# Kernel tuning notes

Measured on AMD Instinct MI355X. Metric: run time of the kernel, lower is better.

The kernel has to match this reference:

```python
import jax, jax.numpy as jnp
import numpy as np

N_NODES = 100000
N_EDGES = 1600000
N_GRAPHS = 4096
IN_DIM, HID, OUT_DIM = 128, 128, 64
BN_EPS = 1e-5


def gcn_conv(x, W, b, src, dst):
    """PyG GCNConv: symmetric norm with self-loops. x:[N,Fin] -> [N,Fout]."""
    h = x @ W  # [N, Fout]
    ones = jnp.ones((src.shape[0],), dtype=h.dtype)
    deg = jax.ops.segment_sum(ones, dst, num_segments=N_NODES) + 1.0  # +1 for self-loop
    dinv = jax.lax.rsqrt(deg)  # deg >= 1, safe
    norm = dinv[src] * dinv[dst]  # [E]
    msg = h[src] * norm[:, None]  # [E, Fout] gather + scale
    agg = jax.ops.segment_sum(msg, dst, num_segments=N_NODES)
    agg = agg + h * (dinv * dinv)[:, None]  # self-loop term, norm = dinv_i^2
    return agg + b


def batchnorm(x, gamma, beta):
    mu = jnp.mean(x, axis=0)
    var = jnp.mean(jnp.square(x - mu), axis=0)  # biased var, torch BN training mode
    return (x - mu) * jax.lax.rsqrt(var + BN_EPS) * gamma + beta


def setup_inputs() -> dict:
    key = jax.random.key(0)
    ks = jax.random.split(key, 12)
    x = jax.random.normal(ks[0], (N_NODES, IN_DIM), dtype=jnp.float32)
    edge_index = jax.random.randint(ks[1], (2, N_EDGES), 0, N_NODES, dtype=jnp.int64)
    batch = jnp.sort(jax.random.randint(ks[2], (N_NODES,), 0, N_GRAPHS, dtype=jnp.int64))
    def lin(k, fi, fo):
        s = 1.0 / np.sqrt(fi)
        return jax.random.uniform(k, (fi, fo), jnp.float32, -s, s)
    return {
        "x": x, "edge_index": edge_index, "batch": batch,
        "W1": lin(ks[3], IN_DIM, HID), "b1": jnp.zeros((HID,), jnp.float32),
        "g1": jnp.ones((HID,), jnp.float32), "be1": jnp.zeros((HID,), jnp.float32),
        "W2": lin(ks[4], HID, HID), "b2": jnp.zeros((HID,), jnp.float32),
        "g2": jnp.ones((HID,), jnp.float32), "be2": jnp.zeros((HID,), jnp.float32),
        "W3": lin(ks[5], HID, HID), "b3": jnp.zeros((HID,), jnp.float32),
        "g3": jnp.ones((HID,), jnp.float32), "be3": jnp.zeros((HID,), jnp.float32),
        "fcW": lin(ks[6], HID, OUT_DIM),
        "fcb": jax.random.uniform(ks[7], (OUT_DIM,), jnp.float32, -1/np.sqrt(HID), 1/np.sqrt(HID)),
    }


def reference(x, edge_index, batch, W1, b1, g1, be1, W2, b2, g2, be2, W3, b3, g3, be3, fcW, fcb):
    src, dst = edge_index[0], edge_index[1]
    h = jax.nn.relu(batchnorm(gcn_conv(x, W1, b1, src, dst), g1, be1))
    h = jax.nn.relu(batchnorm(gcn_conv(h, W2, b2, src, dst), g2, be2))
    h = jax.nn.relu(batchnorm(gcn_conv(h, W3, b3, src, dst), g3, be3))
    # global mean pool over graphs
    sums = jax.ops.segment_sum(h, batch, num_segments=N_GRAPHS)  # [G, HID]
    cnt = jax.ops.segment_sum(jnp.ones((N_NODES,), h.dtype), batch, num_segments=N_GRAPHS)
    pooled = sums / jnp.maximum(cnt, 1.0)[:, None]
    return pooled @ fcW + fcb
```

## Files before the change

### kernel.cpp

```cpp
#include <hip/hip_runtime.h>

#define NN 100000
#define NE 1600000
#define NG 4096
#define HID 128
#define ODIM 64
#define BN_EPS 1e-5f
#define NBUK 782
#define BPAD 896
#define NZROW 256
#define CHUNK 16384
#define PREP_HIST 256
#define PREP_GOFF 17
#define PREP_W 192

typedef unsigned int u32;
typedef unsigned short u16;
typedef short short8 __attribute__((ext_vector_type(8)));
typedef float f32x4 __attribute__((ext_vector_type(4)));

__device__ inline u32 pack_bf16(float a, float b) {
  u32 ua = __float_as_uint(a), ub = __float_as_uint(b);
  ua += 0x7fffu + ((ua >> 16) & 1u);
  ub += 0x7fffu + ((ub >> 16) & 1u);
  return (ua >> 16) | (ub & 0xffff0000u);
}
__device__ inline u16 bf16_of(float v) {
  u32 ua = __float_as_uint(v);
  ua += 0x7fffu + ((ua >> 16) & 1u);
  return (u16)(ua >> 16);
}
__device__ inline float bf_lo(u32 u) { return __uint_as_float(u << 16); }
__device__ inline float bf_hi(u32 u) { return __uint_as_float(u & 0xffff0000u); }

__global__ __launch_bounds__(256) void k_prep(const int* __restrict__ ei, int* __restrict__ bcnt,
                                              const int* __restrict__ batch, int* __restrict__ goff,
                                              const float* __restrict__ W1, const float* __restrict__ W2,
                                              const float* __restrict__ W3, u16* __restrict__ Wt1,
                                              u16* __restrict__ Wt2, u16* __restrict__ Wt3) {
  __shared__ int h[NBUK];
  int b = blockIdx.x, t = threadIdx.x;
  if (b < PREP_HIST) {
    for (int i = t; i < NBUK; i += 256) h[i] = 0;
    __syncthreads();
    const int stride = PREP_HIST * 256;
    for (int e = b * 256 + t; e < NE; e += stride)
      atomicAdd(&h[ei[NE + e] >> 7], 1);
    __syncthreads();
    for (int i = t; i < NBUK; i += 256)
      if (h[i]) atomicAdd(&bcnt[i], h[i]);
  } else if (b < PREP_HIST + PREP_GOFF) {
    int g = (b - PREP_HIST) * 256 + t;
    if (g <= NG) {
      int lo = 0, hi = NN;
      while (lo < hi) { int mid = (lo + hi) >> 1; if (batch[mid] < g) lo = mid + 1; else hi = mid; }
      goff[g] = lo;
    }
  } else {
    int idx = (b - PREP_HIST - PREP_GOFF) * 256 + t;
    int mat = idx >> 14;
    int rem = idx & 16383;
    int n = rem >> 7, k = rem & 127;
    const float* W = (mat == 0) ? W1 : (mat == 1) ? W2 : W3;
    u16* Wt = (mat == 0) ? Wt1 : (mat == 1) ? Wt2 : Wt3;
    Wt[(n << 7) + k] = bf16_of(W[(k << 7) + n]);
  }
}

__global__ __launch_bounds__(1024) void k_bscan(const int* __restrict__ bcnt, int* __restrict__ bboff,
                                                int* __restrict__ bcur) {
  __shared__ int ls[1024];
  int t = threadIdx.x;
  ls[t] = (t < NBUK) ? bcnt[t] : 0;
  __syncthreads();
  for (int d = 1; d < 1024; d <<= 1) {
    int v = 0;
    if (t >= d) v = ls[t - d];
    __syncthreads();
    ls[t] += v;
    __syncthreads();
  }
  if (t < NBUK) {
    int ex = (t == 0) ? 0 : ls[t - 1];
    bboff[t] = ex;
    bcur[t] = ex;
  }
  if (t == 0) bboff[NBUK] = NE;
}

__global__ __launch_bounds__(1024) void k_bscatter(const int* __restrict__ ei, int* __restrict__ bcur,
                                                   u32* __restrict__ ebuf) {
  __shared__ int cnt[NBUK], rnk[NBUK], base[NBUK];
  int t = threadIdx.x;
  int e0 = blockIdx.x * CHUNK;
  for (int i = t; i < NBUK; i += 1024) { cnt[i] = 0; rnk[i] = 0; }
  __syncthreads();
  for (int i = t; i < CHUNK; i += 1024) {
    int e = e0 + i;
    if (e < NE) atomicAdd(&cnt[ei[NE + e] >> 7], 1);
  }
  __syncthreads();
  for (int i = t; i < NBUK; i += 1024) {
    int c = cnt[i];
    base[i] = c ? atomicAdd(&bcur[i], c) : 0;
  }
  __syncthreads();
  for (int i = t; i < CHUNK; i += 1024) {
    int e = e0 + i;
    if (e < NE) {
      int s = ei[e], d = ei[NE + e];
      int b = d >> 7;
      int r = atomicAdd(&rnk[b], 1);
      ebuf[base[b] + r] = ((u32)(d & 127) << 17) | (u32)s;
    }
  }
}

__global__ __launch_bounds__(256) void k_csr(const u32* __restrict__ ebuf, const int* __restrict__ bboff,
                                             int* __restrict__ off, int* __restrict__ oend,
                                             float* __restrict__ dinv, u32* __restrict__ csrc) {
  __shared__ int cnt[128], scn[128], cur[128];
  int b = blockIdx.x, t = threadIdx.x;
  int n0 = b << 7;
  int ebeg = bboff[b], eend = bboff[b + 1];
  int pboff = ebeg + BPAD * b;
  if (t < 128) cnt[t] = 0;
  __syncthreads();
  for (int e = ebeg + t; e < eend; e += 256) atomicAdd(&cnt[ebuf[e] >> 17], 1);
  __syncthreads();
  int pc = 0;
  if (t < 128) { pc = (cnt[t] + 7) & ~7; scn[t] = pc; }
  __syncthreads();
  for (int d = 1; d < 128; d <<= 1) {
    int v = 0;
    if (t >= d && t < 128) v = scn[t - d];
    __syncthreads();
    if (t < 128) scn[t] += v;
    __syncthreads();
  }
  int nvalid = min(128, NN - n0);
  if (t < 128) {
    int ex = scn[t] - pc;
    cur[t] = ex;
    if (t < nvalid) {
      off[n0 + t] = pboff + ex;
      oend[n0 + t] = pboff + scn[t];
      dinv[n0 + t] = rsqrtf((float)cnt[t] + 1.0f);
    }
  }
  __syncthreads();
  for (int e = ebeg + t; e < eend; e += 256) {
    u32 p = ebuf[e];
    int d = p >> 17;
    int pos = pboff + atomicAdd(&cur[d], 1);
    csrc[pos] = p & 0x1ffffu;
  }
  if (t < 128) {
    int ex = scn[t] - pc;
    for (int i = cnt[t]; i < pc; ++i)
      csrc[pboff + ex + i] = (u32)(NN + ((n0 + t + i) & (NZROW - 1)));
  }
}

__global__ __launch_bounds__(256) void k_gemm1(const float* __restrict__ A, const u16* __restrict__ Wt,
                                               const float* __restrict__ dinv, u16* __restrict__ H) {
  __shared__ u16 Ct[128][128];
  u16 (*At)[32] = (u16 (*)[32])(&Ct[0][0]);
  u16 (*Bt)[32] = (u16 (*)[32])(&Ct[32][0]);

  int t = threadIdx.x;
  int w = t >> 6, l = t & 63;
  int quad = l >> 4, lid = l & 15;
  int row0 = blockIdx.x * 128;

  f32x4 acc[2][8];
#pragma unroll
  for (int mt = 0; mt < 2; ++mt)
#pragma unroll
    for (int nt = 0; nt < 8; ++nt) acc[mt][nt] = (f32x4){0.f, 0.f, 0.f, 0.f};

  int ar = t >> 1;
  int ac = (t & 1) << 4;
  int grow = row0 + ar;
  bool aok = grow < NN;

  for (int k0 = 0; k0 < HID; k0 += 32) {
    float4 f0 = {0, 0, 0, 0}, f1 = {0, 0, 0, 0}, f2 = {0, 0, 0, 0}, f3 = {0, 0, 0, 0};
    if (aok) {
      const float4* ap = (const float4*)(A + (size_t)grow * HID + k0 + ac);
      f0 = ap[0]; f1 = ap[1]; f2 = ap[2]; f3 = ap[3];
    }
    uint4 q0, q1;
    q0.x = pack_bf16(f0.x, f0.y); q0.y = pack_bf16(f0.z, f0.w);
    q0.z = pack_bf16(f1.x, f1.y); q0.w = pack_bf16(f1.z, f1.w);
    q1.x = pack_bf16(f2.x, f2.y); q1.y = pack_bf16(f2.z, f2.w);
    q1.z = pack_bf16(f3.x, f3.y); q1.w = pack_bf16(f3.z, f3.w);
    *(uint4*)&At[ar][ac] = q0;
    *(uint4*)&At[ar][ac + 8] = q1;
    const u16* wp = Wt + (size_t)(t >> 1) * HID + k0 + ac;
    *(uint4*)&Bt[t >> 1][ac]     = ((const uint4*)wp)[0];
    *(uint4*)&Bt[t >> 1][ac + 8] = ((const uint4*)wp)[1];
    __syncthreads();
    short8 a0 = *(const short8*)&At[(w << 5) + lid][quad << 3];
    short8 a1 = *(const short8*)&At[(w << 5) + 16 + lid][quad << 3];
#pragma unroll
    for (int nt = 0; nt < 8; ++nt) {
      short8 b = *(const short8*)&Bt[(nt << 4) + lid][quad << 3];
      acc[0][nt] = __builtin_amdgcn_mfma_f32_16x16x32_bf16(a0, b, acc[0][nt], 0, 0, 0);
      acc[1][nt] = __builtin_amdgcn_mfma_f32_16x16x32_bf16(a1, b, acc[1][nt], 0, 0, 0);
    }
    __syncthreads();
  }

  int valid = min(128, NN - row0);
#pragma unroll
  for (int mt = 0; mt < 2; ++mt) {
#pragma unroll
    for (int r = 0; r < 4; ++r) {
      int rl = (w << 5) + (mt << 4) + (quad << 2) + r;
      float dv = (rl < valid) ? dinv[row0 + rl] : 0.f;
#pragma unroll
      for (int nt = 0; nt < 8; ++nt) {
        Ct[rl][(nt << 4) + lid] = bf16_of(acc[mt][nt][r] * dv);
      }
    }
  }
  __syncthreads();
  u16* Hb = H + (size_t)row0 * HID;
  int tot = valid << 4;
  for (int idx = t; idx < tot; idx += 256) {
    ((uint4*)Hb)[idx] = ((const uint4*)Ct)[idx];
  }
}

__device__ inline u32 bn_pair(u32 v, float2 sc, float2 sh) {
  float a = fmaxf(fmaf(bf_lo(v), sc.x, sh.x), 0.f);
  float b = fmaxf(fmaf(bf_hi(v), sc.y, sh.y), 0.f);
  return pack_bf16(a, b);
}

__global__ __launch_bounds__(256) void k_gemm_b(const u16* __restrict__ A, const u16* __restrict__ Wt,
                                                const float* __restrict__ sums, const float* __restrict__ g,
                                                const float* __restrict__ be,
                                                const float* __restrict__ dinv, u16* __restrict__ H) {
  __shared__ u16 Ct[128][128];
  u16 (*At)[32] = (u16 (*)[32])(&Ct[0][0]);
  u16 (*Bt)[32] = (u16 (*)[32])(&Ct[32][0]);
  float* scsh = (float*)&Ct[64][0];

  int t = threadIdx.x;
  int w = t >> 6, l = t & 63;
  int quad = l >> 4, lid = l & 15;
  int row0 = blockIdx.x * 128;

  if (t < 128) {
    const float invN = 1.0f / (float)NN;
    float mu = sums[t] * invN;
    float var = sums[HID + t] * invN - mu * mu;
    float sc = g[t] * rsqrtf(var + BN_EPS);
    scsh[t] = sc;
    scsh[128 + t] = be[t] - mu * sc;
  }

  f32x4 acc[2][8];
#pragma unroll
  for (int mt = 0; mt < 2; ++mt)
#pragma unroll
    for (int nt = 0; nt < 8; ++nt) acc[mt][nt] = (f32x4){0.f, 0.f, 0.f, 0.f};

  int ar = t >> 1;
  int ac = (t & 1) << 4;
  int grow = row0 + ar;
  bool aok = grow < NN;
  __syncthreads();

  for (int k0 = 0; k0 < HID; k0 += 32) {
    uint4 q0 = {0, 0, 0, 0}, q1 = {0, 0, 0, 0};
    if (aok) {
      const uint4* ap = (const uint4*)(A + (size_t)grow * HID + k0 + ac);
      q0 = ap[0]; q1 = ap[1];
    }
    const float2* scp = (const float2*)(scsh + k0 + ac);
    const float2* shp = (const float2*)(scsh + 128 + k0 + ac);
    q0.x = bn_pair(q0.x, scp[0], shp[0]); q0.y = bn_pair(q0.y, scp[1], shp[1]);
    q0.z = bn_pair(q0.z, scp[2], shp[2]); q0.w = bn_pair(q0.w, scp[3], shp[3]);
    q1.x = bn_pair(q1.x, scp[4], shp[4]); q1.y = bn_pair(q1.y, scp[5], shp[5]);
    q1.z = bn_pair(q1.z, scp[6], shp[6]); q1.w = bn_pair(q1.w, scp[7], shp[7]);
    *(uint4*)&At[ar][ac] = q0;
    *(uint4*)&At[ar][ac + 8] = q1;
    const u16* wp = Wt + (size_t)(t >> 1) * HID + k0 + ac;
    *(uint4*)&Bt[t >> 1][ac]     = ((const uint4*)wp)[0];
    *(uint4*)&Bt[t >> 1][ac + 8] = ((const uint4*)wp)[1];
    __syncthreads();
    short8 a0 = *(const short8*)&At[(w << 5) + lid][quad << 3];
    short8 a1 = *(const short8*)&At[(w << 5) + 16 + lid][quad << 3];
#pragma unroll
    for (int nt = 0; nt < 8; ++nt) {
      short8 b = *(const short8*)&Bt[(nt << 4) + lid][quad << 3];
      acc[0][nt] = __builtin_amdgcn_mfma_f32_16x16x32_bf16(a0, b, acc[0][nt], 0, 0, 0);
      acc[1][nt] = __builtin_amdgcn_mfma_f32_16x16x32_bf16(a1, b, acc[1][nt], 0, 0, 0);
    }
    __syncthreads();
  }

  int valid = min(128, NN - row0);
#pragma unroll
  for (int mt = 0; mt < 2; ++mt) {
#pragma unroll
    for (int r = 0; r < 4; ++r) {
      int rl = (w << 5) + (mt << 4) + (quad << 2) + r;
      float dv = (rl < valid) ? dinv[row0 + rl] : 0.f;
#pragma unroll
      for (int nt = 0; nt < 8; ++nt) {
        Ct[rl][(nt << 4) + lid] = bf16_of(acc[mt][nt][r] * dv);
      }
    }
  }
  __syncthreads();
  u16* Hb = H + (size_t)row0 * HID;
  int tot = valid << 4;
  for (int idx = t; idx < tot; idx += 256) {
    ((uint4*)Hb)[idx] = ((const uint4*)Ct)[idx];
  }
}

__global__ __launch_bounds__(256) void k_agg(const u16* __restrict__ h2, const int* __restrict__ off,
                                             const int* __restrict__ oend, const u32* __restrict__ csrc,
                                             const float* __restrict__ dinv, u16* __restrict__ aggb) {
  int node = (int)((blockIdx.x * 256 + threadIdx.x) >> 6);
  int lane = threadIdx.x & 63;
  if (node >= NN) return;
  int beg = off[node], end = oend[node];
  u32 us = ((const u32*)(h2 + (size_t)node * HID))[lane];
  float ax = bf_lo(us), ay = bf_hi(us);
  for (int e = beg; e < end; e += 8) {
    u32 s[8], v[8];
#pragma unroll
    for (int i = 0; i < 8; ++i) s[i] = csrc[e + i];
#pragma unroll
    for (int i = 0; i < 8; ++i) v[i] = ((const u32*)(h2 + (size_t)s[i] * HID))[lane];
#pragma unroll
    for (int i = 0; i < 8; ++i) { ax += bf_lo(v[i]); ay += bf_hi(v[i]); }
  }
  float di = dinv[node];
  ((u32*)(aggb + (size_t)node * HID))[lane] = pack_bf16(ax * di, ay * di);
}

__global__ __launch_bounds__(256) void k_bnstats(const u16* __restrict__ X, float* __restrict__ buf) {
  __shared__ float lsx[256], lssx[256], lsy[256], lssy[256];
  int t = threadIdx.x;
  int colp = t & 63, grp = t >> 6;
  int rbeg = blockIdx.x * 256, rend = min(rbeg + 256, NN);
  float sx = 0.f, ssx = 0.f, sy = 0.f, ssy = 0.f;
  for (int r = rbeg + grp; r < rend; r += 4) {
    u32 v = ((const u32*)(X + (size_t)r * HID))[colp];
    float a = bf_lo(v), b = bf_hi(v);
    sx += a; ssx = fmaf(a, a, ssx);
    sy += b; ssy = fmaf(b, b, ssy);
  }
  lsx[t] = sx; lssx[t] = ssx; lsy[t] = sy; lssy[t] = ssy;
  __syncthreads();
  if (t < 64) {
    sx = lsx[t] + lsx[t + 64] + lsx[t + 128] + lsx[t + 192];
    ssx = lssx[t] + lssx[t + 64] + lssx[t + 128] + lssx[t + 192];
    sy = lsy[t] + lsy[t + 64] + lsy[t + 128] + lsy[t + 192];
    ssy = lssy[t] + lssy[t + 64] + lssy[t + 128] + lssy[t + 192];
    atomicAdd(&buf[2 * colp], sx);
    atomicAdd(&buf[2 * colp + 1], sy);
    atomicAdd(&buf[HID + 2 * colp], ssx);
    atomicAdd(&buf[HID + 2 * colp + 1], ssy);
  }
}

__global__ __launch_bounds__(256) void k_poolfc(const u16* __restrict__ aggb, const float* __restrict__ sums,
                                                const float* __restrict__ g3, const float* __restrict__ be3,
                                                const int* __restrict__ goff, const float* __restrict__ fcW,
                                                const float* __restrict__ fcb, float* __restrict__ out) {
  __shared__ float ls[4][128];
  int t = threadIdx.x;
  int w = t >> 6, lane = t & 63;
  int gr = blockIdx.x * 4 + w;
  const float invN = 1.0f / (float)NN;
  int f0 = lane << 1, f1 = f0 + 1;
  float mu0 = sums[f0] * invN, mu1 = sums[f1] * invN;
  float v0 = sums[HID + f0] * invN - mu0 * mu0;
  float v1 = sums[HID + f1] * invN - mu1 * mu1;
  float sc0 = g3[f0] * rsqrtf(v0 + BN_EPS), sc1 = g3[f1] * rsqrtf(v1 + BN_EPS);
  float sh0 = be3[f0] - mu0 * sc0, sh1 = be3[f1] - mu1 * sc1;
  int beg = goff[gr], end = goff[gr + 1];
  float ax = 0.f, ay = 0.f;
  for (int r = beg; r < end; ++r) {
    u32 v = ((const u32*)(aggb + (size_t)r * HID))[lane];
    ax += fmaxf(fmaf(bf_lo(v), sc0, sh0), 0.f);
    ay += fmaxf(fmaf(bf_hi(v), sc1, sh1), 0.f);
  }
  float inv = 1.0f / fmaxf((float)(end - beg), 1.0f);
  ls[w][f0] = ax * inv;
  ls[w][f1] = ay * inv;
  __syncthreads();
  float acc = fcb[lane];
#pragma unroll 8
  for (int k = 0; k < HID; ++k) acc = fmaf(ls[w][k], fcW[(size_t)k * ODIM + lane], acc);
  out[(size_t)gr * ODIM + lane] = acc;
}

extern "C" void kernel_launch(void* const* d_in, const int* in_sizes, int n_in,
                              void* d_out, int out_size, void* d_ws, size_t ws_size,
                              hipStream_t stream) {
  const float* x     = (const float*)d_in[0];
  const int*   ei    = (const int*)d_in[1];
  const int*   batch = (const int*)d_in[2];
  const float* W1    = (const float*)d_in[3];
  const float* g1    = (const float*)d_in[5];
  const float* be1   = (const float*)d_in[6];
  const float* W2    = (const float*)d_in[7];
  const float* g2    = (const float*)d_in[9];
  const float* be2   = (const float*)d_in[10];
  const float* W3    = (const float*)d_in[11];
  const float* g3    = (const float*)d_in[13];
  const float* be3   = (const float*)d_in[14];
  const float* fcW   = (const float*)d_in[15];
  const float* fcb   = (const float*)d_in[16];
  float* out = (float*)d_out;

  char* p = (char*)d_ws;
  auto alloc = [&](size_t bytes) { char* r = p; p += (bytes + 255) & ~(size_t)255; return r; };
  int*   bcnt   = (int*)alloc((size_t)NBUK * 4);
  float* bnb    = (float*)alloc(3 * 256 * 4);
  size_t zbytes = (size_t)(p - (char*)d_ws);
  int*   bboff  = (int*)alloc((size_t)(NBUK + 1) * 4);
  int*   bcur   = (int*)alloc((size_t)NBUK * 4);
  int*   off    = (int*)alloc((size_t)NN * 4);
  int*   oend   = (int*)alloc((size_t)NN * 4);
  float* dinv   = (float*)alloc((size_t)NN * 4);
  u32*   ebuf   = (u32*)alloc((size_t)NE * 4);
  u32*   csrc   = (u32*)alloc(((size_t)NE + (size_t)BPAD * NBUK) * 4);
  int*   goff   = (int*)alloc((size_t)(NG + 1) * 4);
  u16*   Wt1    = (u16*)alloc((size_t)HID * HID * 2);
  u16*   Wt2    = (u16*)alloc((size_t)HID * HID * 2);
  u16*   Wt3    = (u16*)alloc((size_t)HID * HID * 2);
  u16*   h2     = (u16*)alloc((size_t)(NN + NZROW) * HID * 2);
  u16*   aggb   = (u16*)alloc((size_t)NN * HID * 2);

  hipMemsetAsync(d_ws, 0, zbytes, stream);
  hipMemsetAsync(h2 + (size_t)NN * HID, 0, (size_t)NZROW * HID * 2, stream);

  const int NB = (NN + 255) / 256;
  const int GB = (NN + 127) / 128;
  const int AGB = NN / 4;
  const int SB = (NE + CHUNK - 1) / CHUNK;

  k_prep<<<PREP_HIST + PREP_GOFF + PREP_W, 256, 0, stream>>>(ei, bcnt, batch, goff, W1, W2, W3, Wt1, Wt2, Wt3);
  k_bscan<<<1, 1024, 0, stream>>>(bcnt, bboff, bcur);
  k_bscatter<<<SB, 1024, 0, stream>>>(ei, bcur, ebuf);
  k_csr<<<NBUK, 256, 0, stream>>>(ebuf, bboff, off, oend, dinv, csrc);

  k_gemm1<<<GB, 256, 0, stream>>>(x, Wt1, dinv, h2);
  k_agg<<<AGB, 256, 0, stream>>>(h2, off, oend, csrc, dinv, aggb);
  k_bnstats<<<NB, 256, 0, stream>>>(aggb, bnb);
  k_gemm_b<<<GB, 256, 0, stream>>>(aggb, Wt2, bnb, g1, be1, dinv, h2);
  k_agg<<<AGB, 256, 0, stream>>>(h2, off, oend, csrc, dinv, aggb);
  k_bnstats<<<NB, 256, 0, stream>>>(aggb, bnb + 256);
  k_gemm_b<<<GB, 256, 0, stream>>>(aggb, Wt3, bnb + 256, g2, be2, dinv, h2);
  k_agg<<<AGB, 256, 0, stream>>>(h2, off, oend, csrc, dinv, aggb);
  k_bnstats<<<NB, 256, 0, stream>>>(aggb, bnb + 512);
  k_poolfc<<<NG / 4, 256, 0, stream>>>(aggb, bnb + 512, g3, be3, goff, fcW, fcb, out);
}
```

Measured before the change: 523.5 us.

## Fuse BN statistics into aggregation and pre-shift CSR indices to byte offsets

Folds the batchnorm sum and sum-of-squares reduction into the aggregation kernel, so each layer no longer needs a separate pass that re-reads the aggregated output. Each wave now handles 8 nodes instead of one, and the edge loop is unrolled by 16 with an 8-wide tail. CSR source indices are stored pre-shifted by the row byte size, which removes the multiply from gather address computation. The trade-off is fewer blocks and more serial work per wave, which lowers parallelism and may hurt latency hiding for the gathers.

```diff
diff --git a/kernel.cpp b/kernel.cpp
--- a/kernel.cpp
+++ b/kernel.cpp
@@ -153,12 +153,12 @@
     u32 p = ebuf[e];
     int d = p >> 17;
     int pos = pboff + atomicAdd(&cur[d], 1);
-    csrc[pos] = p & 0x1ffffu;
+    csrc[pos] = (p & 0x1ffffu) << 8;
   }
   if (t < 128) {
     int ex = scn[t] - pc;
     for (int i = cnt[t]; i < pc; ++i)
-      csrc[pboff + ex + i] = (u32)(NN + ((n0 + t + i) & (NZROW - 1)));
+      csrc[pboff + ex + i] = (u32)(NN + ((n0 + t + i) & (NZROW - 1))) << 8;
   }
 }
 
@@ -326,49 +326,57 @@
 
 __global__ __launch_bounds__(256) void k_agg(const u16* __restrict__ h2, const int* __restrict__ off,
                                              const int* __restrict__ oend, const u32* __restrict__ csrc,
-                                             const float* __restrict__ dinv, u16* __restrict__ aggb) {
-  int node = (int)((blockIdx.x * 256 + threadIdx.x) >> 6);
-  int lane = threadIdx.x & 63;
-  if (node >= NN) return;
-  int beg = off[node], end = oend[node];
-  u32 us = ((const u32*)(h2 + (size_t)node * HID))[lane];
-  float ax = bf_lo(us), ay = bf_hi(us);
-  for (int e = beg; e < end; e += 8) {
-    u32 s[8], v[8];
-#pragma unroll
-    for (int i = 0; i < 8; ++i) s[i] = csrc[e + i];
-#pragma unroll
-    for (int i = 0; i < 8; ++i) v[i] = ((const u32*)(h2 + (size_t)s[i] * HID))[lane];
-#pragma unroll
-    for (int i = 0; i < 8; ++i) { ax += bf_lo(v[i]); ay += bf_hi(v[i]); }
-  }
-  float di = dinv[node];
-  ((u32*)(aggb + (size_t)node * HID))[lane] = pack_bf16(ax * di, ay * di);
-}
-
-__global__ __launch_bounds__(256) void k_bnstats(const u16* __restrict__ X, float* __restrict__ buf) {
-  __shared__ float lsx[256], lssx[256], lsy[256], lssy[256];
-  int t = threadIdx.x;
-  int colp = t & 63, grp = t >> 6;
-  int rbeg = blockIdx.x * 256, rend = min(rbeg + 256, NN);
+                                             const float* __restrict__ dinv, u16* __restrict__ aggb,
+                                             float* __restrict__ bnbO) {
+  __shared__ float r0[4][64], r1[4][64], r2[4][64], r3[4][64];
+  int t = threadIdx.x;
+  int wv = t >> 6, lane = t & 63;
+  const char* h2b = (const char*)h2;
+  char* agb = (char*)aggb;
+  u32 lb = (u32)lane << 2;
+  int node0 = (blockIdx.x * 4 + wv) << 3;
   float sx = 0.f, ssx = 0.f, sy = 0.f, ssy = 0.f;
-  for (int r = rbeg + grp; r < rend; r += 4) {
-    u32 v = ((const u32*)(X + (size_t)r * HID))[colp];
-    float a = bf_lo(v), b = bf_hi(v);
-    sx += a; ssx = fmaf(a, a, ssx);
-    sy += b; ssy = fmaf(b, b, ssy);
-  }
-  lsx[t] = sx; lssx[t] = ssx; lsy[t] = sy; lssy[t] = ssy;
+  for (int ni = 0; ni < 8; ++ni) {
+    int node = node0 + ni;
+    int beg = off[node], end = oend[node];
+    u32 us = *(const u32*)(h2b + (((u32)node << 8) + lb));
+    float ax = bf_lo(us), ay = bf_hi(us);
+    int e = beg;
+    for (; e + 16 <= end; e += 16) {
+      u32 s[16], v[16];
+#pragma unroll
+      for (int i = 0; i < 16; ++i) s[i] = csrc[e + i];
+#pragma unroll
+      for (int i = 0; i < 16; ++i) v[i] = *(const u32*)(h2b + (size_t)(s[i] + lb));
+#pragma unroll
+      for (int i = 0; i < 16; ++i) { ax += bf_lo(v[i]); ay += bf_hi(v[i]); }
+    }
+    if (e < end) {
+      u32 s[8], v[8];
+#pragma unroll
+      for (int i = 0; i < 8; ++i) s[i] = csrc[e + i];
+#pragma unroll
+      for (int i = 0; i < 8; ++i) v[i] = *(const u32*)(h2b + (size_t)(s[i] + lb));
+#pragma unroll
+      for (int i = 0; i < 8; ++i) { ax += bf_lo(v[i]); ay += bf_hi(v[i]); }
+    }
+    float di = dinv[node];
+    float axd = ax * di, ayd = ay * di;
+    *(u32*)(agb + (((u32)node << 8) + lb)) = pack_bf16(axd, ayd);
+    sx += axd; ssx = fmaf(axd, axd, ssx);
+    sy += ayd; ssy = fmaf(ayd, ayd, ssy);
+  }
+  r0[wv][lane] = sx; r1[wv][lane] = ssx; r2[wv][lane] = sy; r3[wv][lane] = ssy;
   __syncthreads();
   if (t < 64) {
-    sx = lsx[t] + lsx[t + 64] + lsx[t + 128] + lsx[t + 192];
-    ssx = lssx[t] + lssx[t + 64] + lssx[t + 128] + lssx[t + 192];
-    sy = lsy[t] + lsy[t + 64] + lsy[t + 128] + lsy[t + 192];
-    ssy = lssy[t] + lssy[t + 64] + lssy[t + 128] + lssy[t + 192];
-    atomicAdd(&buf[2 * colp], sx);
-    atomicAdd(&buf[2 * colp + 1], sy);
-    atomicAdd(&buf[HID + 2 * colp], ssx);
-    atomicAdd(&buf[HID + 2 * colp + 1], ssy);
+    float a = r0[0][t] + r0[1][t] + r0[2][t] + r0[3][t];
+    float b = r1[0][t] + r1[1][t] + r1[2][t] + r1[3][t];
+    float c = r2[0][t] + r2[1][t] + r2[2][t] + r2[3][t];
+    float d = r3[0][t] + r3[1][t] + r3[2][t] + r3[3][t];
+    atomicAdd(&bnbO[2 * t], a);
+    atomicAdd(&bnbO[2 * t + 1], c);
+    atomicAdd(&bnbO[HID + 2 * t], b);
+    atomicAdd(&bnbO[HID + 2 * t + 1], d);
   }
 }
 
@@ -445,9 +453,8 @@
   hipMemsetAsync(d_ws, 0, zbytes, stream);
   hipMemsetAsync(h2 + (size_t)NN * HID, 0, (size_t)NZROW * HID * 2, stream);
 
-  const int NB = (NN + 255) / 256;
   const int GB = (NN + 127) / 128;
-  const int AGB = NN / 4;
+  const int AGB = NN / 32;
   const int SB = (NE + CHUNK - 1) / CHUNK;
 
   k_prep<<<PREP_HIST + PREP_GOFF + PREP_W, 256, 0, stream>>>(ei, bcnt, batch, goff, W1, W2, W3, Wt1, Wt2, Wt3);
@@ -456,13 +463,10 @@
   k_csr<<<NBUK, 256, 0, stream>>>(ebuf, bboff, off, oend, dinv, csrc);
 
   k_gemm1<<<GB, 256, 0, stream>>>(x, Wt1, dinv, h2);
-  k_agg<<<AGB, 256, 0, stream>>>(h2, off, oend, csrc, dinv, aggb);
-  k_bnstats<<<NB, 256, 0, stream>>>(aggb, bnb);
+  k_agg<<<AGB, 256, 0, stream>>>(h2, off, oend, csrc, dinv, aggb, bnb);
   k_gemm_b<<<GB, 256, 0, stream>>>(aggb, Wt2, bnb, g1, be1, dinv, h2);
-  k_agg<<<AGB, 256, 0, stream>>>(h2, off, oend, csrc, dinv, aggb);
-  k_bnstats<<<NB, 256, 0, stream>>>(aggb, bnb + 256);
+  k_agg<<<AGB, 256, 0, stream>>>(h2, off, oend, csrc, dinv, aggb, bnb + 256);
   k_gemm_b<<<GB, 256, 0, stream>>>(aggb, Wt3, bnb + 256, g2, be2, dinv, h2);
-  k_agg<<<AGB, 256, 0, stream>>>(h2, off, oend, csrc, dinv, aggb);
-  k_bnstats<<<NB, 256, 0, stream>>>(aggb, bnb + 512);
+  k_agg<<<AGB, 256, 0, stream>>>(h2, off, oend, csrc, dinv, aggb, bnb + 512);
   k_poolfc<<<NG / 4, 256, 0, stream>>>(aggb, bnb + 512, g3, be3, goff, fcW, fcb, out);
 }
```

Result: slower. 795.4 us (+51.9%).
